# Optimization experiments

Measured on AMD Instinct MI355X. Metric: run time of the kernel, lower is better.

## Reference

```python
import jax, jax.numpy as jnp
import numpy as np

M = 6            # num posenc frequencies
K0 = -3
WIDTH = 128
DEPTH = 7
N_PTS = 131072
N_ANNEAL = 0.6 * 5000.0   # self.N = 0.6 * max_iter
PI = 3.14                 # module uses literal 3.14, not math.pi


def _linear_init(key, fan_in, fan_out):
    k1, k2 = jax.random.split(key)
    lim = 1.0 / np.sqrt(fan_in)
    W = jax.random.uniform(k1, (fan_out, fan_in), jnp.float32, -lim, lim)
    b = jax.random.uniform(k2, (fan_out,), jnp.float32, -lim, lim)
    return W, b


def setup_inputs() -> dict:
    key = jax.random.key(0)
    ks = jax.random.split(key, 11)
    dim_x = M * 6 + 3  # 39
    W_in, b_in = _linear_init(ks[0], dim_x, WIDTH)
    hw, hb = [], []
    for i in range(DEPTH - 1):
        W, b = _linear_init(ks[1 + i], WIDTH, WIDTH)
        hw.append(W)
        hb.append(b)
    Ws, bs = jnp.stack(hw), jnp.stack(hb)  # [6,128,128], [6,128]
    Ww, bw = _linear_init(ks[7], WIDTH, 3)
    Wv, bv = _linear_init(ks[8], WIDTH, 3)
    x = jax.random.normal(ks[9], (N_PTS, 3), jnp.float32)
    return {"x": x, "W_in": W_in, "b_in": b_in, "Ws": Ws, "bs": bs,
            "Ww": Ww, "bw": bw, "Wv": Wv, "bv": bv, "iter": 2500}


def _posenc(pos, it):
    # pos: [N,3]
    j = jnp.arange(M, dtype=pos.dtype)
    a = M * it / N_ANNEAL
    w_a = (1.0 - jnp.cos(jnp.clip(a - j, 0.0, 1.0) * PI)) * 0.5      # [M]
    mul = (2.0 ** (j + K0)) * PI                                     # [M]
    ang = pos[..., :, None] * mul                                    # [N,3,M]
    sin = jnp.sin(ang) * w_a
    cos = jnp.cos(ang) * w_a
    # order: sinx,cosx,siny,cosy,sinz,cosz -> [N,3,2,M] flattened
    code = jnp.stack([sin, cos], axis=-2).reshape(pos.shape[0], 6 * M)
    return jnp.concatenate([pos, code], axis=-1)                     # [N,3+6M]


def _skew(w):
    z = jnp.zeros_like(w[..., 0])
    return jnp.stack([
        jnp.stack([z, -w[..., 2], w[..., 1]], -1),
        jnp.stack([w[..., 2], z, -w[..., 0]], -1),
        jnp.stack([-w[..., 1], w[..., 0], z], -1)], -2)              # [N,3,3]


def _exp_se3(w, v, theta):
    # w,v: [N,3] (axis and v/theta), theta: [N,1]
    W = _skew(w)
    W2 = W @ W
    th = theta[..., None]                                            # [N,1,1]
    s, c = jnp.sin(th), jnp.cos(th)
    I = jnp.eye(3, dtype=w.dtype)
    R = I + s * W + (1.0 - c) * W2
    G = I * th + (1.0 - c) * W + (th - s) * W2
    t = G @ v[..., None]                                             # [N,3,1]
    return R, t


def _warp(x, it, W_in, b_in, Ws, bs, Ww, bw, Wv, bv):
    fea = _posenc(x, it)
    fea = jax.nn.leaky_relu(fea @ W_in.T + b_in, 0.01)

    def layer(f, Wb):
        W, b = Wb
        return jax.nn.relu(f @ W.T + b), None

    fea, _ = jax.lax.scan(layer, fea, (Ws, bs))
    w = fea @ Ww.T + bw
    v = fea @ Wv.T + bv
    theta = jnp.linalg.norm(w, axis=-1, keepdims=True)
    w = w / theta
    v = v / theta
    R, t = _exp_se3(w, v, theta)
    return (R @ x[..., None] + t)[..., 0]                            # [N,3]


def reference(x, W_in, b_in, Ws, bs, Ww, bw, Wv, bv, iter):
    it = float(iter)
    warped = _warp(x, it, W_in, b_in, Ws, bs, Ww, bw, Wv, bv)
    # jacobian of sum over batch -> [3, N, 3]; transpose -> [N, 3, 3]
    f_sum = lambda xx: _warp(xx, it, W_in, b_in, Ws, bs, Ww, bw, Wv, bv).sum(0)
    J = jnp.transpose(jax.jacrev(f_sum)(x), (1, 0, 2))
    return warped, J
```

## Files before the change

kernel.cpp:

```cpp
#include <hip/hip_runtime.h>
#include <math.h>

#define NPTS    131072
#define PPB     64
#define THREADS 256
#define NBLK    (NPTS / PPB)
#define HOFF    (7 * 16384)
#define HSZ     (32 * 128)

typedef __attribute__((ext_vector_type(8)))  short short8;
typedef __attribute__((ext_vector_type(16))) float f32x16;
typedef __attribute__((ext_vector_type(2)))  short s16x2;
typedef __attribute__((ext_vector_type(2)))  __bf16 bf16x2v;

union b8cv { short8 v; unsigned u[4]; };

__device__ __forceinline__ unsigned short f2bf(float f) {
  unsigned u = __float_as_uint(f);
  unsigned r = (u + 0x7fffu + ((u >> 16) & 1u)) >> 16;
  return (unsigned short)r;
}
__device__ __forceinline__ unsigned pk2(float lo, float hi) {
  bf16x2v t;
  t[0] = (__bf16)lo;
  t[1] = (__bf16)hi;
  unsigned u; __builtin_memcpy(&u, &t, 4); return u;
}
__device__ __forceinline__ void gld16(const unsigned short* g, unsigned short* l) {
  __builtin_amdgcn_global_load_lds(
      (const __attribute__((address_space(1))) unsigned int*)(g),
      (__attribute__((address_space(3))) unsigned int*)(l), 16, 0, 0);
}
__device__ __forceinline__ float qbcast0(float v) {
  return __int_as_float(
      __builtin_amdgcn_mov_dpp(__float_as_int(v), 0x000, 0xf, 0xf, true));
}
__device__ __forceinline__ unsigned relu_pk(unsigned p) {
  unsigned vs = (unsigned)__builtin_amdgcn_mov_dpp((int)p, 0x000, 0xf, 0xf, true);
  s16x2 m2; __builtin_memcpy(&m2, &vs, 4);
  m2 = m2 >> 15;
  unsigned m; __builtin_memcpy(&m, &m2, 4);
  unsigned r;
  asm("v_bfi_b32 %0, %1, 0, %2" : "=v"(r) : "v"(m), "v"(p));
  return r;
}
__device__ __forceinline__ void cross3(const float a[3], const float b[3], float o[3]) {
  o[0] = a[1]*b[2] - a[2]*b[1];
  o[1] = a[2]*b[0] - a[0]*b[2];
  o[2] = a[0]*b[1] - a[1]*b[0];
}
__device__ __forceinline__ float dot3(const float a[3], const float b[3]) {
  return a[0]*b[0] + a[1]*b[1] + a[2]*b[2];
}

__global__ void convert_weights(const float* __restrict__ W_in,
                                const float* __restrict__ b_in,
                                const float* __restrict__ Ws,
                                const float* __restrict__ bs,
                                const float* __restrict__ Ww,
                                const float* __restrict__ Wv,
                                unsigned short* __restrict__ wsW) {
  int idx = blockIdx.x * 256 + threadIdx.x;
  if (idx >= HOFF + HSZ) return;
  float v;
  if (idx < HOFF) {
    int l = idx >> 14, r = idx & 16383, c = r >> 7, k = r & 127;
    if (l == 0) {
      if (k < 39) {
        v = W_in[c * 39 + k];
      } else if (k >= 64 && c < 14) {
        int j  = c * 64 + (k - 64);
        int lb = j >> 7, rr = j & 127;
        int mt = rr >> 5, rd = rr & 31;
        int e2 = rd & 3, hh = (rd >> 2) & 1, q = rd >> 3;
        int src = 32*mt + 16*(q>>1) + 8*hh + 4*(q&1) + e2;
        v = (lb == 0) ? b_in[src] : bs[(lb - 1) * 128 + src];
      } else {
        v = 0.0f;
      }
    } else {
      v = Ws[(l - 1) * 16384 + c * 128 + k];
    }
  } else {
    int r = idx - HOFF, o = r >> 7, k = r & 127;
    v = (o < 3) ? Ww[o * 128 + k] : (o < 6) ? Wv[(o - 3) * 128 + k] : 0.0f;
  }
  wsW[idx] = f2bf(v);
}

__device__ __forceinline__ void dma_half(const unsigned short* __restrict__ g,
                                         unsigned short* lds, int tid) {
  #pragma unroll
  for (int i = 0; i < 4; ++i) {
    int flat = i * 256 + tid;
    int R = flat >> 4, chs = flat & 15, ch = chs ^ (R & 15);
    gld16(g + R * 128 + ch * 8, lds + flat * 8);
  }
}

__device__ __forceinline__ short8 bias_af(const unsigned short* __restrict__ bb,
                                          int off, int c32) {
  b8cv cv;
  cv.u[0] = (unsigned)bb[off + c32];
  cv.u[1] = 0; cv.u[2] = 0; cv.u[3] = 0;
  return cv.v;
}

template <bool LEAKY>
__device__ __forceinline__ void act_pack(const f32x16 (&acc)[2], short8* dst) {
  #pragma unroll
  for (int mt = 0; mt < 2; ++mt)
    #pragma unroll
    for (int qh = 0; qh < 2; ++qh) {
      b8cv cv;
      #pragma unroll
      for (int qs = 0; qs < 2; ++qs) {
        int q = 2*qh + qs;
        if (LEAKY) {
          float pr[4];
          #pragma unroll
          for (int e2 = 0; e2 < 4; ++e2) {
            float post = acc[mt][4*q + e2];
            float vraw = qbcast0(post);
            pr[e2] = vraw > 0.0f ? post : post * 0.01f;
          }
          cv.u[2*qs]     = pk2(pr[0], pr[1]);
          cv.u[2*qs + 1] = pk2(pr[2], pr[3]);
        } else {
          cv.u[2*qs]     = relu_pk(pk2(acc[mt][4*q+0], acc[mt][4*q+1]));
          cv.u[2*qs + 1] = relu_pk(pk2(acc[mt][4*q+2], acc[mt][4*q+3]));
        }
      }
      dst[2*mt + qh] = cv.v;
    }
}

template <int NKS, bool LEAKY, bool HASNEXT>
__device__ __forceinline__ void mlp_layer(short8 (&pgA)[8], short8 (&pgB)[8],
                                          const unsigned short* s0s,
                                          const unsigned short* s1s,
                                          unsigned short* s0w, unsigned short* s1w,
                                          const int (&aoff)[8],
                                          const unsigned short* __restrict__ bb,
                                          const short8 bind, const f32x16& Z,
                                          const unsigned short* __restrict__ Wthis,
                                          const unsigned short* __restrict__ Wnext,
                                          int tid, int c32) {
  dma_half(Wthis + 64 * 128, s1w, tid);

  short8 tA[4], tB[4];

  {
    f32x16 aA[2], aB[2];
    short8 bf0 = bias_af(bb,  64, c32);
    short8 bf1 = bias_af(bb,  96, c32);
    aA[0] = __builtin_amdgcn_mfma_f32_32x32x16_bf16(bf0, bind, Z, 0, 0, 0);
    aB[0] = __builtin_amdgcn_mfma_f32_32x32x16_bf16(bf0, bind, Z, 0, 0, 0);
    aA[1] = __builtin_amdgcn_mfma_f32_32x32x16_bf16(bf1, bind, Z, 0, 0, 0);
    aB[1] = __builtin_amdgcn_mfma_f32_32x32x16_bf16(bf1, bind, Z, 0, 0, 0);
    #pragma unroll
    for (int ks = 0; ks < NKS; ++ks) {
      #pragma unroll
      for (int m = 0; m < 2; ++m) {
        short8 af = *(const short8*)(s0s + m * 4096 + aoff[ks]);
        aA[m] = __builtin_amdgcn_mfma_f32_32x32x16_bf16(af, pgA[ks], aA[m], 0, 0, 0);
        aB[m] = __builtin_amdgcn_mfma_f32_32x32x16_bf16(af, pgB[ks], aB[m], 0, 0, 0);
      }
    }
    act_pack<LEAKY>(aA, tA);
    act_pack<LEAKY>(aB, tB);
  }

  __syncthreads();
  if (HASNEXT) dma_half(Wnext, s0w, tid);

  {
    f32x16 aA[2], aB[2];
    short8 bf2 = bias_af(bb, 192, c32);
    short8 bf3 = bias_af(bb, 224, c32);
    aA[0] = __builtin_amdgcn_mfma_f32_32x32x16_bf16(bf2, bind, Z, 0, 0, 0);
    aB[0] = __builtin_amdgcn_mfma_f32_32x32x16_bf16(bf2, bind, Z, 0, 0, 0);
    aA[1] = __builtin_amdgcn_mfma_f32_32x32x16_bf16(bf3, bind, Z, 0, 0, 0);
    aB[1] = __builtin_amdgcn_mfma_f32_32x32x16_bf16(bf3, bind, Z, 0, 0, 0);
    #pragma unroll
    for (int ks = 0; ks < NKS; ++ks) {
      #pragma unroll
      for (int m = 0; m < 2; ++m) {
        short8 af = *(const short8*)(s1s + m * 4096 + aoff[ks]);
        aA[m] = __builtin_amdgcn_mfma_f32_32x32x16_bf16(af, pgA[ks], aA[m], 0, 0, 0);
        aB[m] = __builtin_amdgcn_mfma_f32_32x32x16_bf16(af, pgB[ks], aB[m], 0, 0, 0);
      }
    }
    act_pack<LEAKY>(aA, &pgA[4]);
    act_pack<LEAKY>(aB, &pgB[4]);
  }

  #pragma unroll
  for (int i = 0; i < 4; ++i) { pgA[i] = tA[i]; pgB[i] = tB[i]; }
  __syncthreads();
}

__device__ __forceinline__ void posenc_pack(const float X[3], int d, int h,
                                            float aM, short8* pg) {
  #pragma unroll
  for (int j = 4; j < 8; ++j) pg[j] = (short8)0;
  #pragma unroll
  for (int j = 0; j < 4; ++j) {
    b8cv cv;
    #pragma unroll
    for (int ii = 0; ii < 4; ++ii) {
      int i = 4*j + ii;
      int mt = i >> 3, rr = i & 7, q = rr >> 1, s = rr & 1;
      int u0 = 32*mt + 16*(q>>1) + 8*h + 4*(q&1) + 2*s;
      float vp[2];
      #pragma unroll
      for (int ci = 0; ci < 2; ++ci) {
        int c = u0 + ci;
        float val = 0.0f;
        if (c < 3) {
          val = (d == 0) ? X[c] : ((c == d - 1) ? 1.0f : 0.0f);
        } else if (c < 39) {
          int kk = c - 3;
          int a  = kk / 12;
          int rm = kk - a * 12;
          int t  = rm / 6;
          int jf = rm - t * 6;
          float e2 = exp2f((float)(jf - 3));
          float mj = e2 * 3.14f;
          float tt = fminf(fmaxf(aM - (float)jf, 0.0f), 1.0f);
          float wj = (1.0f - __builtin_amdgcn_cosf(tt * 0.49974652f)) * 0.5f;
          float rev = X[a] * (e2 * 0.49974652f);
          float fr  = rev - floorf(rev);
          float sv = __builtin_amdgcn_sinf(fr);
          float cvv = __builtin_amdgcn_cosf(fr);
          if (d == 0)          val = (t == 0 ? sv : cvv) * wj;
          else if (a == d - 1) val = (t == 0 ? cvv : -sv) * (mj * wj);
        }
        vp[ci] = val;
      }
      cv.u[ii] = pk2(vp[0], vp[1]);
    }
    pg[j] = cv.v;
  }
}

__global__ __launch_bounds__(THREADS, 2)
void nerfies_mfma(const float* __restrict__ x,
                  const float* __restrict__ bw,
                  const float* __restrict__ bv,
                  const unsigned short* __restrict__ wsW,
                  const int* __restrict__ iterp,
                  float* __restrict__ out)
{
  __shared__ __align__(16) unsigned short sWl[2][64 * 128];
  float* sH = (float*)sWl[1];

  const int tid  = threadIdx.x;
  const int lane = tid & 63;
  const int wv   = tid >> 6;
  const int c32  = lane & 31;
  const int h    = lane >> 5;
  const int p0   = blockIdx.x * PPB;
  const int sig  = (c32 & 0x13) | ((c32 & 4) << 1) | ((c32 & 8) >> 1);

  dma_half(wsW, sWl[0], tid);

  int aoff[8];
  #pragma unroll
  for (int ks = 0; ks < 8; ++ks) aoff[ks] = ((2*ks + h) ^ (sig & 15)) << 3;
  const unsigned short* s0s = sWl[0] + sig * 128;
  const unsigned short* s1s = sWl[1] + sig * 128;

  f32x16 Z;
  #pragma unroll
  for (int e = 0; e < 16; ++e) Z[e] = 0.0f;
  short8 bind;
  {
    b8cv cv;
    cv.u[0] = ((c32 & 3) == 0) ? 0x3F00u : 0u;
    cv.u[1] = 0; cv.u[2] = 0; cv.u[3] = 0;
    bind = cv.v;
  }

  const int d   = c32 & 3;
  const int gpA = p0 + wv * 16 + (c32 >> 2);
  const int gpB = gpA + 8;
  float XA[3] = { x[gpA * 3 + 0], x[gpA * 3 + 1], x[gpA * 3 + 2] };
  float XB[3] = { x[gpB * 3 + 0], x[gpB * 3 + 1], x[gpB * 3 + 2] };

  int iraw = iterp[0];
  float it = (iraw > 0 && iraw < 100000000) ? (float)iraw : ((const float*)iterp)[0];
  const float aM = 6.0f * it / 3000.0f;

  short8 pgA[8], pgB[8];
  posenc_pack(XA, d, h, aM, pgA);
  posenc_pack(XB, d, h, aM, pgB);
  __syncthreads();

  mlp_layer<3, true , true >(pgA, pgB, s0s, s1s, sWl[0], sWl[1], aoff, wsW + 0*256, bind, Z, wsW + 0*16384, wsW + 1*16384, tid, c32);
  mlp_layer<8, false, true >(pgA, pgB, s0s, s1s, sWl[0], sWl[1], aoff, wsW + 1*256, bind, Z, wsW + 1*16384, wsW + 2*16384, tid, c32);
  mlp_layer<8, false, true >(pgA, pgB, s0s, s1s, sWl[0], sWl[1], aoff, wsW + 2*256, bind, Z, wsW + 2*16384, wsW + 3*16384, tid, c32);
  mlp_layer<8, false, true >(pgA, pgB, s0s, s1s, sWl[0], sWl[1], aoff, wsW + 3*256, bind, Z, wsW + 3*16384, wsW + 4*16384, tid, c32);
  mlp_layer<8, false, true >(pgA, pgB, s0s, s1s, sWl[0], sWl[1], aoff, wsW + 4*256, bind, Z, wsW + 4*16384, wsW + 5*16384, tid, c32);
  mlp_layer<8, false, true >(pgA, pgB, s0s, s1s, sWl[0], sWl[1], aoff, wsW + 5*256, bind, Z, wsW + 5*16384, wsW + 6*16384, tid, c32);
  mlp_layer<8, false, false>(pgA, pgB, s0s, s1s, sWl[0], sWl[1], aoff, wsW + 6*256, bind, Z, wsW + 6*16384, wsW,           tid, c32);

  {
    const unsigned short* hw = wsW + HOFF;
    short8 af0 = *(const short8*)(hw + c32 * 128 + 8 * h);
    f32x16 hA = __builtin_amdgcn_mfma_f32_32x32x16_bf16(af0, pgA[0], Z, 0, 0, 0);
    f32x16 hB = __builtin_amdgcn_mfma_f32_32x32x16_bf16(af0, pgB[0], Z, 0, 0, 0);
    #pragma unroll
    for (int ks = 1; ks < 8; ++ks) {
      short8 afrag = *(const short8*)(hw + c32 * 128 + ks * 16 + 8 * h);
      hA = __builtin_amdgcn_mfma_f32_32x32x16_bf16(afrag, pgA[ks], hA, 0, 0, 0);
      hB = __builtin_amdgcn_mfma_f32_32x32x16_bf16(afrag, pgB[ks], hB, 0, 0, 0);
    }
    int rgA = wv * 64 + c32;
    int rgB = rgA + 32;
    if (h == 0) {
      *(float4*)(sH + rgA * 8) = make_float4(hA[0], hA[1], hA[2], hA[3]);
      *(float4*)(sH + rgB * 8) = make_float4(hB[0], hB[1], hB[2], hB[3]);
    } else {
      *(float2*)(sH + rgA * 8 + 4) = make_float2(hA[0], hA[1]);
      *(float2*)(sH + rgB * 8 + 4) = make_float2(hB[0], hB[1]);
    }
  }
  __syncthreads();

  if (lane < 16) {
    const int p   = lane;
    const int g   = p >> 3, pi = p & 7;
    const int gpp = p0 + wv * 16 + p;
    const int rb  = wv * 64 + g * 32 + pi * 4;
    float XX[3] = { x[gpp*3+0], x[gpp*3+1], x[gpp*3+2] };
    float w[3], v[3], dw[3][3], dv[3][3];
    #pragma unroll
    for (int i = 0; i < 3; ++i) {
      w[i] = sH[rb * 8 + i]     + bw[i];
      v[i] = sH[rb * 8 + 3 + i] + bv[i];
      #pragma unroll
      for (int dd = 0; dd < 3; ++dd) {
        dw[dd][i] = sH[(rb + 1 + dd) * 8 + i];
        dv[dd][i] = sH[(rb + 1 + dd) * 8 + 3 + i];
      }
    }
    float th  = sqrtf(w[0]*w[0] + w[1]*w[1] + w[2]*w[2]);
    float ith = 1.0f / th;
    float u[3]  = { w[0]*ith, w[1]*ith, w[2]*ith };
    float vh[3] = { v[0]*ith, v[1]*ith, v[2]*ith };
    float s = sinf(th), c = cosf(th);
    float C2 = 1.0f - c;
    float ths = th - s;
    float uxx[3]; cross3(u, XX, uxx);
    float udx = dot3(u, XX);
    float uxv[3]; cross3(u, vh, uxv);
    float udv = dot3(u, vh);
    #pragma unroll
    for (int i = 0; i < 3; ++i) {
      float Rx = XX[i] + s * uxx[i] + C2 * (u[i] * udx - XX[i]);
      float tt = th * vh[i] + C2 * uxv[i] + ths * (u[i] * udv - vh[i]);
      out[gpp*3 + i] = Rx + tt;
    }
    float* Jout = out + (size_t)NPTS * 3 + (size_t)gpp * 9;
    #pragma unroll
    for (int dd = 0; dd < 3; ++dd) {
      float dwv[3] = { dw[dd][0], dw[dd][1], dw[dd][2] };
      float dvv[3] = { dv[dd][0], dv[dd][1], dv[dd][2] };
      float dth = dot3(w, dwv) * ith;
      float du[3], dvhv[3];
      #pragma unroll
      for (int i = 0; i < 3; ++i) {
        du[i]   = (dwv[i] - u[i]  * dth) * ith;
        dvhv[i] = (dvv[i] - vh[i] * dth) * ith;
      }
      float ex[3] = { dd == 0 ? 1.0f : 0.0f, dd == 1 ? 1.0f : 0.0f, dd == 2 ? 1.0f : 0.0f };
      float dsv  = c  * dth;
      float dC2  = s  * dth;
      float dths = C2 * dth;
      float duxx[3]; cross3(du, XX, duxx);
      float uxe[3];  cross3(u, ex, uxe);
      float dudx = dot3(du, XX) + u[dd];
      float duxv[3]; cross3(du, vh, duxv);
      float uxdv[3]; cross3(u, dvhv, uxdv);
      float dudv = dot3(du, vh) + dot3(u, dvhv);
      #pragma unroll
      for (int i = 0; i < 3; ++i) {
        float dRx = ex[i] + dsv * uxx[i] + s * (duxx[i] + uxe[i])
                  + dC2 * (u[i] * udx - XX[i])
                  + C2 * (du[i] * udx + u[i] * dudx - ex[i]);
        float dt  = dth * vh[i] + th * dvhv[i] + dC2 * uxv[i]
                  + C2 * (duxv[i] + uxdv[i])
                  + dths * (u[i] * udv - vh[i])
                  + ths * (du[i] * udv + u[i] * dudv - dvhv[i]);
        Jout[i * 3 + dd] = dRx + dt;
      }
    }
  }
}

extern "C" void kernel_launch(void* const* d_in, const int* in_sizes, int n_in,
                              void* d_out, int out_size, void* d_ws, size_t ws_size,
                              hipStream_t stream) {
  const float* x    = (const float*)d_in[0];
  const float* W_in = (const float*)d_in[1];
  const float* b_in = (const float*)d_in[2];
  const float* Ws   = (const float*)d_in[3];
  const float* bs   = (const float*)d_in[4];
  const float* Ww   = (const float*)d_in[5];
  const float* bw   = (const float*)d_in[6];
  const float* Wv   = (const float*)d_in[7];
  const float* bv   = (const float*)d_in[8];
  const int*   itp  = (const int*)d_in[9];
  unsigned short* wsW = (unsigned short*)d_ws;

  convert_weights<<<dim3((HOFF + HSZ + 255) / 256), dim3(256), 0, stream>>>(
      W_in, b_in, Ws, bs, Ww, Wv, wsW);
  nerfies_mfma<<<dim3(NBLK), dim3(THREADS), 0, stream>>>(
      x, bw, bv, wsW, itp, (float*)d_out);
}
```

Before: 186.6 us.

## Read MLP weight fragments directly from global memory instead of LDS staging

Removes the double-buffered async global-to-LDS weight copies and the per-layer block barriers. Each wave now loads its bf16 weight fragments straight from global memory (L1/L2 cached), and LDS shrinks to a small head buffer. This removes the sync stalls and frees LDS, which may allow more blocks per CU. In exchange, every wave fetches the full weights redundantly through the cache with scattered 16-byte loads, and there is no explicit prefetch to overlap that latency.

```diff
diff --git a/kernel.cpp b/kernel.cpp
--- a/kernel.cpp
+++ b/kernel.cpp
@@ -25,11 +25,6 @@
   t[0] = (__bf16)lo;
   t[1] = (__bf16)hi;
   unsigned u; __builtin_memcpy(&u, &t, 4); return u;
-}
-__device__ __forceinline__ void gld16(const unsigned short* g, unsigned short* l) {
-  __builtin_amdgcn_global_load_lds(
-      (const __attribute__((address_space(1))) unsigned int*)(g),
-      (__attribute__((address_space(3))) unsigned int*)(l), 16, 0, 0);
 }
 __device__ __forceinline__ float qbcast0(float v) {
   return __int_as_float(
@@ -88,16 +83,6 @@
   wsW[idx] = f2bf(v);
 }
 
-__device__ __forceinline__ void dma_half(const unsigned short* __restrict__ g,
-                                         unsigned short* lds, int tid) {
-  #pragma unroll
-  for (int i = 0; i < 4; ++i) {
-    int flat = i * 256 + tid;
-    int R = flat >> 4, chs = flat & 15, ch = chs ^ (R & 15);
-    gld16(g + R * 128 + ch * 8, lds + flat * 8);
-  }
-}
-
 __device__ __forceinline__ short8 bias_af(const unsigned short* __restrict__ bb,
                                           int off, int c32) {
   b8cv cv;
@@ -135,19 +120,12 @@
     }
 }
 
-template <int NKS, bool LEAKY, bool HASNEXT>
+template <int NKS, bool LEAKY>
 __device__ __forceinline__ void mlp_layer(short8 (&pgA)[8], short8 (&pgB)[8],
-                                          const unsigned short* s0s,
-                                          const unsigned short* s1s,
-                                          unsigned short* s0w, unsigned short* s1w,
-                                          const int (&aoff)[8],
+                                          const unsigned short* __restrict__ pW,
                                           const unsigned short* __restrict__ bb,
                                           const short8 bind, const f32x16& Z,
-                                          const unsigned short* __restrict__ Wthis,
-                                          const unsigned short* __restrict__ Wnext,
-                                          int tid, int c32) {
-  dma_half(Wthis + 64 * 128, s1w, tid);
-
+                                          int c32) {
   short8 tA[4], tB[4];
 
   {
@@ -162,7 +140,7 @@
     for (int ks = 0; ks < NKS; ++ks) {
       #pragma unroll
       for (int m = 0; m < 2; ++m) {
-        short8 af = *(const short8*)(s0s + m * 4096 + aoff[ks]);
+        short8 af = *(const short8*)(pW + m * 4096 + ks * 16);
         aA[m] = __builtin_amdgcn_mfma_f32_32x32x16_bf16(af, pgA[ks], aA[m], 0, 0, 0);
         aB[m] = __builtin_amdgcn_mfma_f32_32x32x16_bf16(af, pgB[ks], aB[m], 0, 0, 0);
       }
@@ -170,9 +148,6 @@
     act_pack<LEAKY>(aA, tA);
     act_pack<LEAKY>(aB, tB);
   }
-
-  __syncthreads();
-  if (HASNEXT) dma_half(Wnext, s0w, tid);
 
   {
     f32x16 aA[2], aB[2];
@@ -186,7 +161,7 @@
     for (int ks = 0; ks < NKS; ++ks) {
       #pragma unroll
       for (int m = 0; m < 2; ++m) {
-        short8 af = *(const short8*)(s1s + m * 4096 + aoff[ks]);
+        short8 af = *(const short8*)(pW + (2 + m) * 4096 + ks * 16);
         aA[m] = __builtin_amdgcn_mfma_f32_32x32x16_bf16(af, pgA[ks], aA[m], 0, 0, 0);
         aB[m] = __builtin_amdgcn_mfma_f32_32x32x16_bf16(af, pgB[ks], aB[m], 0, 0, 0);
       }
@@ -197,7 +172,6 @@
 
   #pragma unroll
   for (int i = 0; i < 4; ++i) { pgA[i] = tA[i]; pgB[i] = tB[i]; }
-  __syncthreads();
 }
 
 __device__ __forceinline__ void posenc_pack(const float X[3], int d, int h,
@@ -252,8 +226,7 @@
                   const int* __restrict__ iterp,
                   float* __restrict__ out)
 {
-  __shared__ __align__(16) unsigned short sWl[2][64 * 128];
-  float* sH = (float*)sWl[1];
+  __shared__ __align__(16) float sH[PPB * 4 * 8];
 
   const int tid  = threadIdx.x;
   const int lane = tid & 63;
@@ -263,13 +236,7 @@
   const int p0   = blockIdx.x * PPB;
   const int sig  = (c32 & 0x13) | ((c32 & 4) << 1) | ((c32 & 8) >> 1);
 
-  dma_half(wsW, sWl[0], tid);
-
-  int aoff[8];
-  #pragma unroll
-  for (int ks = 0; ks < 8; ++ks) aoff[ks] = ((2*ks + h) ^ (sig & 15)) << 3;
-  const unsigned short* s0s = sWl[0] + sig * 128;
-  const unsigned short* s1s = sWl[1] + sig * 128;
+  const unsigned short* pW = wsW + sig * 128 + h * 8;
 
   f32x16 Z;
   #pragma unroll
@@ -295,15 +262,14 @@
   short8 pgA[8], pgB[8];
   posenc_pack(XA, d, h, aM, pgA);
   posenc_pack(XB, d, h, aM, pgB);
-  __syncthreads();
-
-  mlp_layer<3, true , true >(pgA, pgB, s0s, s1s, sWl[0], sWl[1], aoff, wsW + 0*256, bind, Z, wsW + 0*16384, wsW + 1*16384, tid, c32);
-  mlp_layer<8, false, true >(pgA, pgB, s0s, s1s, sWl[0], sWl[1], aoff, wsW + 1*256, bind, Z, wsW + 1*16384, wsW + 2*16384, tid, c32);
-  mlp_layer<8, false, true >(pgA, pgB, s0s, s1s, sWl[0], sWl[1], aoff, wsW + 2*256, bind, Z, wsW + 2*16384, wsW + 3*16384, tid, c32);
-  mlp_layer<8, false, true >(pgA, pgB, s0s, s1s, sWl[0], sWl[1], aoff, wsW + 3*256, bind, Z, wsW + 3*16384, wsW + 4*16384, tid, c32);
-  mlp_layer<8, false, true >(pgA, pgB, s0s, s1s, sWl[0], sWl[1], aoff, wsW + 4*256, bind, Z, wsW + 4*16384, wsW + 5*16384, tid, c32);
-  mlp_layer<8, false, true >(pgA, pgB, s0s, s1s, sWl[0], sWl[1], aoff, wsW + 5*256, bind, Z, wsW + 5*16384, wsW + 6*16384, tid, c32);
-  mlp_layer<8, false, false>(pgA, pgB, s0s, s1s, sWl[0], sWl[1], aoff, wsW + 6*256, bind, Z, wsW + 6*16384, wsW,           tid, c32);
+
+  mlp_layer<3, true >(pgA, pgB, pW + 0*16384, wsW + 0*256, bind, Z, c32);
+  mlp_layer<8, false>(pgA, pgB, pW + 1*16384, wsW + 1*256, bind, Z, c32);
+  mlp_layer<8, false>(pgA, pgB, pW + 2*16384, wsW + 2*256, bind, Z, c32);
+  mlp_layer<8, false>(pgA, pgB, pW + 3*16384, wsW + 3*256, bind, Z, c32);
+  mlp_layer<8, false>(pgA, pgB, pW + 4*16384, wsW + 4*256, bind, Z, c32);
+  mlp_layer<8, false>(pgA, pgB, pW + 5*16384, wsW + 5*256, bind, Z, c32);
+  mlp_layer<8, false>(pgA, pgB, pW + 6*16384, wsW + 6*256, bind, Z, c32);
 
   {
     const unsigned short* hw = wsW + HOFF;
```

After: 276.8 us. 1.48x slower.

## Double-buffer full layer weights in LDS and prefetch next layer during compute

Applied to the files above, without the earlier changes.

Replaces the half-layer weight streaming, which used two syncs per layer, with full 128x128 weight buffers in LDS. The next layer's weights are prefetched into the other buffer while the current layer computes, leaving one barrier per layer. Bias MFMAs are shared between the A and B accumulators, and the zero accumulator is built inline instead of held in registers. LDS use doubles to 64KB per block, which can lower occupancy with two blocks per CU.

```diff
diff --git a/kernel.cpp b/kernel.cpp
--- a/kernel.cpp
+++ b/kernel.cpp
@@ -30,6 +30,12 @@
   __builtin_amdgcn_global_load_lds(
       (const __attribute__((address_space(1))) unsigned int*)(g),
       (__attribute__((address_space(3))) unsigned int*)(l), 16, 0, 0);
+}
+__device__ __forceinline__ f32x16 zf() {
+  f32x16 z;
+  #pragma unroll
+  for (int e = 0; e < 16; ++e) z[e] = 0.0f;
+  return z;
 }
 __device__ __forceinline__ float qbcast0(float v) {
   return __int_as_float(
@@ -88,10 +94,10 @@
   wsW[idx] = f2bf(v);
 }
 
-__device__ __forceinline__ void dma_half(const unsigned short* __restrict__ g,
+__device__ __forceinline__ void dma_full(const unsigned short* __restrict__ g,
                                          unsigned short* lds, int tid) {
   #pragma unroll
-  for (int i = 0; i < 4; ++i) {
+  for (int i = 0; i < 8; ++i) {
     int flat = i * 256 + tid;
     int R = flat >> 4, chs = flat & 15, ch = chs ^ (R & 15);
     gld16(g + R * 128 + ch * 8, lds + flat * 8);
@@ -137,32 +143,32 @@
 
 template <int NKS, bool LEAKY, bool HASNEXT>
 __device__ __forceinline__ void mlp_layer(short8 (&pgA)[8], short8 (&pgB)[8],
-                                          const unsigned short* s0s,
-                                          const unsigned short* s1s,
-                                          unsigned short* s0w, unsigned short* s1w,
+                                          const unsigned short* scur,
+                                          unsigned short* snxt,
                                           const int (&aoff)[8],
                                           const unsigned short* __restrict__ bb,
-                                          const short8 bind, const f32x16& Z,
-                                          const unsigned short* __restrict__ Wthis,
+                                          const short8 bind,
                                           const unsigned short* __restrict__ Wnext,
                                           int tid, int c32) {
-  dma_half(Wthis + 64 * 128, s1w, tid);
+  if (HASNEXT) dma_full(Wnext, snxt, tid);
 
   short8 tA[4], tB[4];
 
   {
     f32x16 aA[2], aB[2];
-    short8 bf0 = bias_af(bb,  64, c32);
-    short8 bf1 = bias_af(bb,  96, c32);
-    aA[0] = __builtin_amdgcn_mfma_f32_32x32x16_bf16(bf0, bind, Z, 0, 0, 0);
-    aB[0] = __builtin_amdgcn_mfma_f32_32x32x16_bf16(bf0, bind, Z, 0, 0, 0);
-    aA[1] = __builtin_amdgcn_mfma_f32_32x32x16_bf16(bf1, bind, Z, 0, 0, 0);
-    aB[1] = __builtin_amdgcn_mfma_f32_32x32x16_bf16(bf1, bind, Z, 0, 0, 0);
-    #pragma unroll
-    for (int ks = 0; ks < NKS; ++ks) {
+    #pragma unroll
+    for (int m = 0; m < 2; ++m) {
+      f32x16 bias = __builtin_amdgcn_mfma_f32_32x32x16_bf16(
+          bias_af(bb, 64 + 32*m, c32), bind, zf(), 0, 0, 0);
+      short8 af0 = *(const short8*)(scur + m * 4096 + aoff[0]);
+      aA[m] = __builtin_amdgcn_mfma_f32_32x32x16_bf16(af0, pgA[0], bias, 0, 0, 0);
+      aB[m] = __builtin_amdgcn_mfma_f32_32x32x16_bf16(af0, pgB[0], bias, 0, 0, 0);
+    }
+    #pragma unroll
+    for (int ks = 1; ks < NKS; ++ks) {
       #pragma unroll
       for (int m = 0; m < 2; ++m) {
-        short8 af = *(const short8*)(s0s + m * 4096 + aoff[ks]);
+        short8 af = *(const short8*)(scur + m * 4096 + aoff[ks]);
         aA[m] = __builtin_amdgcn_mfma_f32_32x32x16_bf16(af, pgA[ks], aA[m], 0, 0, 0);
         aB[m] = __builtin_amdgcn_mfma_f32_32x32x16_bf16(af, pgB[ks], aB[m], 0, 0, 0);
       }
@@ -171,22 +177,21 @@
     act_pack<LEAKY>(aB, tB);
   }
 
-  __syncthreads();
-  if (HASNEXT) dma_half(Wnext, s0w, tid);
-
   {
     f32x16 aA[2], aB[2];
-    short8 bf2 = bias_af(bb, 192, c32);
-    short8 bf3 = bias_af(bb, 224, c32);
-    aA[0] = __builtin_amdgcn_mfma_f32_32x32x16_bf16(bf2, bind, Z, 0, 0, 0);
-    aB[0] = __builtin_amdgcn_mfma_f32_32x32x16_bf16(bf2, bind, Z, 0, 0, 0);
-    aA[1] = __builtin_amdgcn_mfma_f32_32x32x16_bf16(bf3, bind, Z, 0, 0, 0);
-    aB[1] = __builtin_amdgcn_mfma_f32_32x32x16_bf16(bf3, bind, Z, 0, 0, 0);
-    #pragma unroll
-    for (int ks = 0; ks < NKS; ++ks) {
+    #pragma unroll
+    for (int m = 0; m < 2; ++m) {
+      f32x16 bias = __builtin_amdgcn_mfma_f32_32x32x16_bf16(
+          bias_af(bb, 192 + 32*m, c32), bind, zf(), 0, 0, 0);
+      short8 af0 = *(const short8*)(scur + (2 + m) * 4096 + aoff[0]);
+      aA[m] = __builtin_amdgcn_mfma_f32_32x32x16_bf16(af0, pgA[0], bias, 0, 0, 0);
+      aB[m] = __builtin_amdgcn_mfma_f32_32x32x16_bf16(af0, pgB[0], bias, 0, 0, 0);
+    }
+    #pragma unroll
+    for (int ks = 1; ks < NKS; ++ks) {
       #pragma unroll
       for (int m = 0; m < 2; ++m) {
-        short8 af = *(const short8*)(s1s + m * 4096 + aoff[ks]);
+        short8 af = *(const short8*)(scur + (2 + m) * 4096 + aoff[ks]);
         aA[m] = __builtin_amdgcn_mfma_f32_32x32x16_bf16(af, pgA[ks], aA[m], 0, 0, 0);
         aB[m] = __builtin_amdgcn_mfma_f32_32x32x16_bf16(af, pgB[ks], aB[m], 0, 0, 0);
       }
@@ -197,7 +202,8 @@
 
   #pragma unroll
   for (int i = 0; i < 4; ++i) { pgA[i] = tA[i]; pgB[i] = tB[i]; }
-  __syncthreads();
+
+  if (HASNEXT) __syncthreads();
 }
 
 __device__ __forceinline__ void posenc_pack(const float X[3], int d, int h,
@@ -252,7 +258,7 @@
                   const int* __restrict__ iterp,
                   float* __restrict__ out)
 {
-  __shared__ __align__(16) unsigned short sWl[2][64 * 128];
+  __shared__ __align__(16) unsigned short sWl[2][128 * 128];
   float* sH = (float*)sWl[1];
 
   const int tid  = threadIdx.x;
@@ -263,7 +269,7 @@
   const int p0   = blockIdx.x * PPB;
   const int sig  = (c32 & 0x13) | ((c32 & 4) << 1) | ((c32 & 8) >> 1);
 
-  dma_half(wsW, sWl[0], tid);
+  dma_full(wsW, sWl[0], tid);
 
   int aoff[8];
   #pragma unroll
@@ -271,9 +277,6 @@
   const unsigned short* s0s = sWl[0] + sig * 128;
   const unsigned short* s1s = sWl[1] + sig * 128;
 
-  f32x16 Z;
-  #pragma unroll
-  for (int e = 0; e < 16; ++e) Z[e] = 0.0f;
   short8 bind;
   {
     b8cv cv;
@@ -297,19 +300,19 @@
   posenc_pack(XB, d, h, aM, pgB);
   __syncthreads();
 
-  mlp_layer<3, true , true >(pgA, pgB, s0s, s1s, sWl[0], sWl[1], aoff, wsW + 0*256, bind, Z, wsW + 0*16384, wsW + 1*16384, tid, c32);
-  mlp_layer<8, false, true >(pgA, pgB, s0s, s1s, sWl[0], sWl[1], aoff, wsW + 1*256, bind, Z, wsW + 1*16384, wsW + 2*16384, tid, c32);
-  mlp_layer<8, false, true >(pgA, pgB, s0s, s1s, sWl[0], sWl[1], aoff, wsW + 2*256, bind, Z, wsW + 2*16384, wsW + 3*16384, tid, c32);
-  mlp_layer<8, false, true >(pgA, pgB, s0s, s1s, sWl[0], sWl[1], aoff, wsW + 3*256, bind, Z, wsW + 3*16384, wsW + 4*16384, tid, c32);
-  mlp_layer<8, false, true >(pgA, pgB, s0s, s1s, sWl[0], sWl[1], aoff, wsW + 4*256, bind, Z, wsW + 4*16384, wsW + 5*16384, tid, c32);
-  mlp_layer<8, false, true >(pgA, pgB, s0s, s1s, sWl[0], sWl[1], aoff, wsW + 5*256, bind, Z, wsW + 5*16384, wsW + 6*16384, tid, c32);
-  mlp_layer<8, false, false>(pgA, pgB, s0s, s1s, sWl[0], sWl[1], aoff, wsW + 6*256, bind, Z, wsW + 6*16384, wsW,           tid, c32);
+  mlp_layer<3, true , true >(pgA, pgB, s0s, sWl[1], aoff, wsW + 0*256, bind, wsW + 1*16384, tid, c32);
+  mlp_layer<8, false, true >(pgA, pgB, s1s, sWl[0], aoff, wsW + 1*256, bind, wsW + 2*16384, tid, c32);
+  mlp_layer<8, false, true >(pgA, pgB, s0s, sWl[1], aoff, wsW + 2*256, bind, wsW + 3*16384, tid, c32);
+  mlp_layer<8, false, true >(pgA, pgB, s1s, sWl[0], aoff, wsW + 3*256, bind, wsW + 4*16384, tid, c32);
+  mlp_layer<8, false, true >(pgA, pgB, s0s, sWl[1], aoff, wsW + 4*256, bind, wsW + 5*16384, tid, c32);
+  mlp_layer<8, false, true >(pgA, pgB, s1s, sWl[0], aoff, wsW + 5*256, bind, wsW + 6*16384, tid, c32);
+  mlp_layer<8, false, false>(pgA, pgB, s0s, sWl[1], aoff, wsW + 6*256, bind, wsW,           tid, c32);
 
   {
     const unsigned short* hw = wsW + HOFF;
     short8 af0 = *(const short8*)(hw + c32 * 128 + 8 * h);
-    f32x16 hA = __builtin_amdgcn_mfma_f32_32x32x16_bf16(af0, pgA[0], Z, 0, 0, 0);
-    f32x16 hB = __builtin_amdgcn_mfma_f32_32x32x16_bf16(af0, pgB[0], Z, 0, 0, 0);
+    f32x16 hA = __builtin_amdgcn_mfma_f32_32x32x16_bf16(af0, pgA[0], zf(), 0, 0, 0);
+    f32x16 hB = __builtin_amdgcn_mfma_f32_32x32x16_bf16(af0, pgB[0], zf(), 0, 0, 0);
     #pragma unroll
     for (int ks = 1; ks < 8; ++ks) {
       short8 afrag = *(const short8*)(hw + c32 * 128 + ks * 16 + 8 * h);
```

Result: no change. 189.2 us (+1.4%).
